# Kernel optimization log

Hardware: AMD Instinct MI355X
Metric: run time of the kernel (lower is better)

The kernel has to match this reference:

```python
import jax, jax.numpy as jnp
import numpy as np

B, S, E, H = 4, 2048, 1024, 16
HD = E // H  # head_dim = 64
EPS = 1.1920928955078125e-07  # torch.finfo(float32).eps (RMSNorm eps=None default)


def _rmsnorm(x, w):
    # normalize over last dim
    ms = jnp.mean(x * x, axis=-1, keepdims=True)
    return x * jax.lax.rsqrt(ms + EPS) * w


def _rope(x, start_pos=0):
    # x: [B, H, S, HD]; interleaved (even/odd) rotary embedding
    seq_len = x.shape[-2]
    inv_freq = 1.0 / (10000.0 ** (jnp.arange(0, HD, 2, dtype=jnp.float32) / HD))  # [HD/2]
    t = jnp.arange(start_pos, start_pos + seq_len, dtype=jnp.float32)  # [S]
    freqs = t[:, None] * inv_freq[None, :]  # [S, HD/2]
    cos = jnp.cos(freqs)[None, None]  # [1,1,S,HD/2]
    sin = jnp.sin(freqs)[None, None]
    x1 = x[..., 0::2]
    x2 = x[..., 1::2]
    o1 = x1 * cos - x2 * sin
    o2 = x1 * sin + x2 * cos
    # stack(..., -1).flatten(-2) -> re-interleave
    return jnp.stack((o1, o2), axis=-1).reshape(x.shape)


def setup_inputs() -> dict:
    key = jax.random.key(0)
    k1, k2, k3, k4 = jax.random.split(key, 4)
    lim = 1.0 / np.sqrt(E)
    return {
        "q": jax.random.normal(k1, (B, S, E), jnp.float32),
        "k": jax.random.normal(k2, (B, S, E), jnp.float32),
        "v": jax.random.normal(k3, (B, S, E), jnp.float32),
        "q_norm_w": jnp.ones((HD,), jnp.float32),
        "k_norm_w": jnp.ones((HD,), jnp.float32),
        "proj_w": jax.random.uniform(k4, (E, E), jnp.float32, -lim, lim),
        "proj_b": jnp.zeros((E,), jnp.float32),
    }


def reference(q, k, v, q_norm_w, k_norm_w, proj_w, proj_b):
    b, s, _ = q.shape
    scale = HD ** -0.5
    # [B,S,E] -> [B,H,S,HD]
    qh = q.reshape(b, s, H, HD).transpose(0, 2, 1, 3)
    kh = k.reshape(b, s, H, HD).transpose(0, 2, 1, 3)
    vh = v.reshape(b, s, H, HD).transpose(0, 2, 1, 3)
    # per-head QK RMSNorm then RoPE
    qh = _rope(_rmsnorm(qh, q_norm_w))
    kh = _rope(_rmsnorm(kh, k_norm_w))
    # explicit attention (no mask path)
    scores = jnp.einsum("bhqd,bhkd->bhqk", qh, kh) * scale  # [B,H,S,S]
    attn = jax.nn.softmax(scores, axis=-1)
    ctx = jnp.einsum("bhqk,bhkd->bhqd", attn, vh)
    ctx = ctx.transpose(0, 2, 1, 3).reshape(b, s, E)
    return ctx @ proj_w.T + proj_b
```

## Files before the change

kernel.cpp:

```cpp
#include <hip/hip_runtime.h>
#include <hip/hip_bf16.h>
#include <cstdint>

#define B_ 4
#define S_ 2048
#define E_ 1024
#define H_ 16
#define HD_ 64
#define EPS_ 1.1920928955078125e-07f

typedef __attribute__((ext_vector_type(8))) short shortx8;
typedef __attribute__((ext_vector_type(4))) float floatx4;
typedef __attribute__((ext_vector_type(8))) _Float16 halfx8;
typedef __attribute__((ext_vector_type(2))) __fp16 fp16x2;

#define C1_ 0.18033688068389154f

__global__ __launch_bounds__(256) void prep(
    const float* __restrict__ q, const float* __restrict__ k,
    const float* __restrict__ v,
    const float* __restrict__ qw, const float* __restrict__ kw,
    const float* __restrict__ pw,
    __hip_bfloat16* __restrict__ qh, __hip_bfloat16* __restrict__ kh,
    _Float16* __restrict__ vt, __hip_bfloat16* __restrict__ wb)
{
    __shared__ _Float16 tile[64][72];
    const int bid = blockIdx.x;
    const int tid = threadIdx.x;

    if (bid < 16384) {
        const size_t PT = (size_t)B_ * S_ * E_ / 4;
        size_t t = (size_t)bid * 256 + tid;
        const bool is_k = (t >= PT);
        if (is_k) t -= PT;

        const int row = (int)(t >> 8);
        const int b   = row / S_;
        const int s   = row % S_;
        const int grp = (int)(t & 255);
        const int h   = grp >> 4;
        const int dl  = (grp & 15) * 4;

        const float* __restrict__ src = is_k ? k : q;
        const float* __restrict__ w   = is_k ? kw : qw;
        __hip_bfloat16* __restrict__ dst = is_k ? kh : qh;

        const float4 x  = ((const float4*)src)[t];
        const float4 wv = ((const float4*)w)[grp & 15];

        float ss = x.x * x.x + x.y * x.y + x.z * x.z + x.w * x.w;
#pragma unroll
        for (int m = 1; m < 16; m <<= 1) ss += __shfl_xor(ss, m);
        float r = rsqrtf(ss * (1.0f / HD_) + EPS_);
        if (!is_k) r *= C1_;

        const float xn0 = x.x * r * wv.x;
        const float xn1 = x.y * r * wv.y;
        const float xn2 = x.z * r * wv.z;
        const float xn3 = x.w * r * wv.w;

        const float L2I = 0.41524101186092029f;
        const int   i0  = dl >> 1;
        const float f0  = (float)s * __builtin_amdgcn_exp2f(-(float)i0 * L2I);
        const float f1  = (float)s * __builtin_amdgcn_exp2f(-(float)(i0 + 1) * L2I);
        const float c0 = __cosf(f0), sn0 = __sinf(f0);
        const float c1 = __cosf(f1), sn1 = __sinf(f1);

        __hip_bfloat16 pk[4];
        pk[0] = __float2bfloat16(xn0 * c0 - xn1 * sn0);
        pk[1] = __float2bfloat16(xn0 * sn0 + xn1 * c0);
        pk[2] = __float2bfloat16(xn2 * c1 - xn3 * sn1);
        pk[3] = __float2bfloat16(xn2 * sn1 + xn3 * c1);
        *(ushort4*)(dst + ((size_t)((b * H_ + h) * S_ + s)) * HD_ + dl) =
            *(const ushort4*)pk;
    } else if (bid < 18432) {
        const int bb2 = bid - 16384;
        const int s0  = (bb2 & 31) * 64;
        const int bh  = bb2 >> 5;
        const int b   = bh >> 4, h = bh & 15;
        {
            const int sl = tid >> 2;
            const int o  = sl;
            const int n  = (o & 32) | (((o >> 2) & 3) << 3) |
                           (((o >> 4) & 1) << 2) | (o & 3);
            const int d0 = (tid & 3) * 16;
            const float* __restrict__ src =
                v + ((size_t)(b * S_ + s0 + sl)) * E_ + h * HD_ + d0;
            float4 f0 = ((const float4*)src)[0];
            float4 f1 = ((const float4*)src)[1];
            float4 f2 = ((const float4*)src)[2];
            float4 f3 = ((const float4*)src)[3];
            float vals[16] = {f0.x,f0.y,f0.z,f0.w, f1.x,f1.y,f1.z,f1.w,
                              f2.x,f2.y,f2.z,f2.w, f3.x,f3.y,f3.z,f3.w};
#pragma unroll
            for (int j = 0; j < 16; ++j)
                tile[d0 + j][n] = (_Float16)vals[j];
        }
        __syncthreads();
        {
            const int d  = tid >> 2;
            const int sg = (tid & 3) * 16;
            _Float16* __restrict__ dst =
                vt + ((size_t)(bh * HD_ + d)) * S_ + s0 + sg;
            ((uint4*)dst)[0] = *(const uint4*)&tile[d][sg];
            ((uint4*)dst)[1] = *(const uint4*)&tile[d][sg + 8];
        }
    } else {
        const int i = (bid - 18432) * 256 + tid;
        float4 f = ((const float4*)pw)[i];
        wb[4 * i + 0] = __float2bfloat16(f.x);
        wb[4 * i + 1] = __float2bfloat16(f.y);
        wb[4 * i + 2] = __float2bfloat16(f.z);
        wb[4 * i + 3] = __float2bfloat16(f.w);
    }
}

__global__ __launch_bounds__(256, 4) void attn(
    const __hip_bfloat16* __restrict__ qh, const __hip_bfloat16* __restrict__ kh,
    const _Float16* __restrict__ vt, __hip_bfloat16* __restrict__ ctx)
{
    __shared__ __hip_bfloat16 Kt[128][72];
    __shared__ _Float16       Vt[64][152];

    const int bid  = blockIdx.x;
    const int slot = bid >> 3;
    const int bh   = ((bid & 7) << 3) | (slot & 7);
    const int q0   = (slot >> 3) * 128;
    const int tid  = threadIdx.x;
    const int wv   = tid >> 6;
    const int lane = tid & 63;
    const int l16  = lane & 15;
    const int quad = lane >> 4;
    const int b    = bh >> 4, h = bh & 15;

    shortx8 aq[2][2];
#pragma unroll
    for (int mh = 0; mh < 2; ++mh) {
        const __hip_bfloat16* qbase =
            qh + ((size_t)bh * S_ + q0 + wv * 32 + mh * 16 + l16) * HD_;
        aq[mh][0] = *(const shortx8*)(qbase + quad * 8);
        aq[mh][1] = *(const shortx8*)(qbase + 32 + quad * 8);
    }

    const halfx8 ones = {(_Float16)1.f, (_Float16)1.f, (_Float16)1.f, (_Float16)1.f,
                         (_Float16)1.f, (_Float16)1.f, (_Float16)1.f, (_Float16)1.f};

    floatx4 O[2][4] = {};
    floatx4 O5[2]   = {};

    const __hip_bfloat16* __restrict__ kbase = kh + (size_t)bh * S_ * HD_;
    const _Float16* __restrict__ vbase = vt + (size_t)bh * HD_ * S_;

    const int sr = tid >> 1, sc = (tid & 1) * 32;
    const int vr = tid >> 2, vc = (tid & 3) * 32;

    for (int kt = 0; kt < S_ / 128; ++kt) {
        {
            const uint4* kp = (const uint4*)(kbase +
                (size_t)(kt * 128 + sr) * HD_ + sc);
            uint4 k0 = kp[0], k1 = kp[1], k2 = kp[2], k3 = kp[3];
            *(uint4*)&Kt[sr][sc]      = k0;
            *(uint4*)&Kt[sr][sc + 8]  = k1;
            *(uint4*)&Kt[sr][sc + 16] = k2;
            *(uint4*)&Kt[sr][sc + 24] = k3;
        }
        {
            const uint4* vp = (const uint4*)(vbase +
                (size_t)vr * S_ + kt * 128 + vc);
            uint4 v0 = vp[0], v1 = vp[1], v2 = vp[2], v3 = vp[3];
            *(uint4*)&Vt[vr][vc]      = v0;
            *(uint4*)&Vt[vr][vc + 8]  = v1;
            *(uint4*)&Vt[vr][vc + 16] = v2;
            *(uint4*)&Vt[vr][vc + 24] = v3;
        }
        __syncthreads();

#pragma unroll
        for (int hk = 0; hk < 2; ++hk) {
            halfx8 bb[2][2];
#pragma unroll
            for (int f = 0; f < 2; ++f) {
                floatx4 s4p[2][2];
                __builtin_amdgcn_s_setprio(1);
#pragma unroll
                for (int nt2 = 0; nt2 < 2; ++nt2) {
                    const int nt = 2 * f + nt2;
                    const shortx8 kb0 =
                        *(const shortx8*)&Kt[hk * 64 + nt * 16 + l16][quad * 8];
                    const shortx8 kb1 =
                        *(const shortx8*)&Kt[hk * 64 + nt * 16 + l16][32 + quad * 8];
#pragma unroll
                    for (int mh = 0; mh < 2; ++mh) {
                        floatx4 c = {0.f, 0.f, 0.f, 0.f};
                        c = __builtin_amdgcn_mfma_f32_16x16x32_bf16(kb0, aq[mh][0], c, 0, 0, 0);
                        c = __builtin_amdgcn_mfma_f32_16x16x32_bf16(kb1, aq[mh][1], c, 0, 0, 0);
                        s4p[mh][nt2] = c;
                    }
                }
                __builtin_amdgcn_s_setprio(0);
#pragma unroll
                for (int mh = 0; mh < 2; ++mh) {
                    union { fp16x2 h2[4]; halfx8 h8; } u;
                    u.h2[0] = __builtin_amdgcn_cvt_pkrtz(
                        __builtin_amdgcn_exp2f(s4p[mh][0][0]),
                        __builtin_amdgcn_exp2f(s4p[mh][0][1]));
                    u.h2[1] = __builtin_amdgcn_cvt_pkrtz(
                        __builtin_amdgcn_exp2f(s4p[mh][0][2]),
                        __builtin_amdgcn_exp2f(s4p[mh][0][3]));
                    u.h2[2] = __builtin_amdgcn_cvt_pkrtz(
                        __builtin_amdgcn_exp2f(s4p[mh][1][0]),
                        __builtin_amdgcn_exp2f(s4p[mh][1][1]));
                    u.h2[3] = __builtin_amdgcn_cvt_pkrtz(
                        __builtin_amdgcn_exp2f(s4p[mh][1][2]),
                        __builtin_amdgcn_exp2f(s4p[mh][1][3]));
                    bb[mh][f] = u.h8;
                }
            }

            __builtin_amdgcn_s_setprio(1);
#pragma unroll
            for (int mh = 0; mh < 2; ++mh) {
                O5[mh] = __builtin_amdgcn_mfma_f32_16x16x32_f16(ones, bb[mh][0], O5[mh], 0, 0, 0);
                O5[mh] = __builtin_amdgcn_mfma_f32_16x16x32_f16(ones, bb[mh][1], O5[mh], 0, 0, 0);
            }

#pragma unroll
            for (int dt = 0; dt < 4; ++dt) {
                const _Float16* vrow = &Vt[dt * 16 + l16][hk * 64];
                const halfx8 A0 = *(const halfx8*)(vrow + quad * 8);
                const halfx8 A1 = *(const halfx8*)(vrow + 32 + quad * 8);
#pragma unroll
                for (int mh = 0; mh < 2; ++mh) {
                    O[mh][dt] = __builtin_amdgcn_mfma_f32_16x16x32_f16(
                        A0, bb[mh][0], O[mh][dt], 0, 0, 0);
                    O[mh][dt] = __builtin_amdgcn_mfma_f32_16x16x32_f16(
                        A1, bb[mh][1], O[mh][dt], 0, 0, 0);
                }
            }
            __builtin_amdgcn_s_setprio(0);
        }
        __syncthreads();
    }

#pragma unroll
    for (int mh = 0; mh < 2; ++mh) {
        const float inv = 1.0f / O5[mh][0];
        const int s = q0 + wv * 32 + mh * 16 + l16;
        __hip_bfloat16* cb = ctx + ((size_t)(b * S_ + s)) * E_ + h * HD_;
#pragma unroll
        for (int dt = 0; dt < 4; ++dt) {
            __hip_bfloat16 pk[4];
#pragma unroll
            for (int r = 0; r < 4; ++r)
                pk[r] = __float2bfloat16(O[mh][dt][r] * inv);
            *(ushort4*)(cb + dt * 16 + quad * 4) = *(const ushort4*)pk;
        }
    }
}

__global__ __launch_bounds__(256) void proj(
    const __hip_bfloat16* __restrict__ ctx, const __hip_bfloat16* __restrict__ wb,
    const float* __restrict__ bias, float* __restrict__ out)
{
    __shared__ __hip_bfloat16 As[128][72];
    __shared__ __hip_bfloat16 Bs[128][72];

    const int bid  = blockIdx.x;
    const int slot = bid >> 3;
    const int mblk = ((bid & 7) << 3) | (slot & 7);
    const int nblk = slot >> 3;
    const int m0 = mblk * 128;
    const int n0 = nblk * 128;
    const int tid  = threadIdx.x;
    const int wv   = tid >> 6;
    const int lane = tid & 63;
    const int l16  = lane & 15;
    const int quad = lane >> 4;
    const int wr   = (wv >> 1) * 64;
    const int wc   = (wv & 1) * 64;

    const int srow = tid >> 1;
    const int scol = (tid & 1) * 32;

    floatx4 acc[4][4] = {};

    for (int k0 = 0; k0 < E_; k0 += 64) {
        const uint4* ap = (const uint4*)(ctx + (size_t)(m0 + srow) * E_ + k0 + scol);
        const uint4* bp = (const uint4*)(wb  + (size_t)(n0 + srow) * E_ + k0 + scol);
        uint4 a0 = ap[0], a1 = ap[1], a2 = ap[2], a3 = ap[3];
        uint4 b0 = bp[0], b1 = bp[1], b2 = bp[2], b3 = bp[3];
        *(uint4*)&As[srow][scol]      = a0;
        *(uint4*)&As[srow][scol + 8]  = a1;
        *(uint4*)&As[srow][scol + 16] = a2;
        *(uint4*)&As[srow][scol + 24] = a3;
        *(uint4*)&Bs[srow][scol]      = b0;
        *(uint4*)&Bs[srow][scol + 8]  = b1;
        *(uint4*)&Bs[srow][scol + 16] = b2;
        *(uint4*)&Bs[srow][scol + 24] = b3;
        __syncthreads();

#pragma unroll
        for (int ks = 0; ks < 2; ++ks) {
            shortx8 af[4], bf[4];
#pragma unroll
            for (int mt = 0; mt < 4; ++mt)
                af[mt] = *(const shortx8*)&As[wr + mt * 16 + l16][ks * 32 + quad * 8];
#pragma unroll
            for (int nt = 0; nt < 4; ++nt)
                bf[nt] = *(const shortx8*)&Bs[wc + nt * 16 + l16][ks * 32 + quad * 8];

#pragma unroll
            for (int mt = 0; mt < 4; ++mt)
#pragma unroll
                for (int nt = 0; nt < 4; ++nt)
                    acc[mt][nt] = __builtin_amdgcn_mfma_f32_16x16x32_bf16(
                        af[mt], bf[nt], acc[mt][nt], 0, 0, 0);
        }
        __syncthreads();
    }

#pragma unroll
    for (int nt = 0; nt < 4; ++nt) {
        const float bv = bias[n0 + wc + nt * 16 + l16];
#pragma unroll
        for (int mt = 0; mt < 4; ++mt)
#pragma unroll
            for (int r = 0; r < 4; ++r) {
                const int mrow = m0 + wr + mt * 16 + quad * 4 + r;
                const int ncol = n0 + wc + nt * 16 + l16;
                out[(size_t)mrow * E_ + ncol] = acc[mt][nt][r] + bv;
            }
    }
}

extern "C" void kernel_launch(void* const* d_in, const int* in_sizes, int n_in,
                              void* d_out, int out_size, void* d_ws, size_t ws_size,
                              hipStream_t stream)
{
    const float* q  = (const float*)d_in[0];
    const float* k  = (const float*)d_in[1];
    const float* v  = (const float*)d_in[2];
    const float* qw = (const float*)d_in[3];
    const float* kw = (const float*)d_in[4];
    const float* pw = (const float*)d_in[5];
    const float* pb = (const float*)d_in[6];
    float* out = (float*)d_out;

    char* ws = (char*)d_ws;
    const size_t SEG = (size_t)B_ * H_ * S_ * HD_ * 2;
    __hip_bfloat16* qh  = (__hip_bfloat16*)(ws);
    __hip_bfloat16* kh  = (__hip_bfloat16*)(ws + SEG);
    _Float16*       vt  = (_Float16*)(ws + 2 * SEG);
    __hip_bfloat16* ctx = (__hip_bfloat16*)(ws + 3 * SEG);
    __hip_bfloat16* wbp = (__hip_bfloat16*)(ws + 4 * SEG);

    prep<<<dim3(19456), 256, 0, stream>>>(q, k, v, qw, kw, pw, qh, kh, vt, wbp);
    attn<<<dim3(1024), 256, 0, stream>>>(qh, kh, vt, ctx);
    proj<<<dim3(512), 256, 0, stream>>>(ctx, wbp, pb, out);
}
```

Measured before the change: 248.1 us.

## Software-pipeline QK, exp and PV stages within each K tile

Replaces the nested hk/f loops with a hand-scheduled sequence that interleaves QK MFMAs, exp2/convert work, and PV MFMAs across four 32-column chunks, so transcendental VALU work overlaps matrix-core work. Also drops the min-blocks-per-CU hint from launch bounds, letting the compiler use more registers for the extra live score buffers. The cost is higher register pressure and possibly lower occupancy.

```diff
diff --git a/kernel.cpp b/kernel.cpp
--- a/kernel.cpp
+++ b/kernel.cpp
@@ -115,7 +115,7 @@
     }
 }
 
-__global__ __launch_bounds__(256, 4) void attn(
+__global__ __launch_bounds__(256) void attn(
     const __hip_bfloat16* __restrict__ qh, const __hip_bfloat16* __restrict__ kh,
     const _Float16* __restrict__ vt, __hip_bfloat16* __restrict__ ctx)
 {
@@ -175,70 +175,88 @@
         }
         __syncthreads();
 
-#pragma unroll
-        for (int hk = 0; hk < 2; ++hk) {
-            halfx8 bb[2][2];
-#pragma unroll
-            for (int f = 0; f < 2; ++f) {
-                floatx4 s4p[2][2];
-                __builtin_amdgcn_s_setprio(1);
-#pragma unroll
-                for (int nt2 = 0; nt2 < 2; ++nt2) {
-                    const int nt = 2 * f + nt2;
-                    const shortx8 kb0 =
-                        *(const shortx8*)&Kt[hk * 64 + nt * 16 + l16][quad * 8];
-                    const shortx8 kb1 =
-                        *(const shortx8*)&Kt[hk * 64 + nt * 16 + l16][32 + quad * 8];
-#pragma unroll
-                    for (int mh = 0; mh < 2; ++mh) {
-                        floatx4 c = {0.f, 0.f, 0.f, 0.f};
-                        c = __builtin_amdgcn_mfma_f32_16x16x32_bf16(kb0, aq[mh][0], c, 0, 0, 0);
-                        c = __builtin_amdgcn_mfma_f32_16x16x32_bf16(kb1, aq[mh][1], c, 0, 0, 0);
-                        s4p[mh][nt2] = c;
-                    }
-                }
-                __builtin_amdgcn_s_setprio(0);
-#pragma unroll
-                for (int mh = 0; mh < 2; ++mh) {
-                    union { fp16x2 h2[4]; halfx8 h8; } u;
-                    u.h2[0] = __builtin_amdgcn_cvt_pkrtz(
-                        __builtin_amdgcn_exp2f(s4p[mh][0][0]),
-                        __builtin_amdgcn_exp2f(s4p[mh][0][1]));
-                    u.h2[1] = __builtin_amdgcn_cvt_pkrtz(
-                        __builtin_amdgcn_exp2f(s4p[mh][0][2]),
-                        __builtin_amdgcn_exp2f(s4p[mh][0][3]));
-                    u.h2[2] = __builtin_amdgcn_cvt_pkrtz(
-                        __builtin_amdgcn_exp2f(s4p[mh][1][0]),
-                        __builtin_amdgcn_exp2f(s4p[mh][1][1]));
-                    u.h2[3] = __builtin_amdgcn_cvt_pkrtz(
-                        __builtin_amdgcn_exp2f(s4p[mh][1][2]),
-                        __builtin_amdgcn_exp2f(s4p[mh][1][3]));
-                    bb[mh][f] = u.h8;
-                }
+        floatx4 sP[2][2], sQ[2][2], sR[2][2], sS[2][2];
+        halfx8 bbA[2], bbB[2], bbC[2], bbD[2];
+
+        auto QKsub = [&](int hk, int nt, floatx4 (&s)[2][2], int nt2) {
+            const shortx8 kb0 =
+                *(const shortx8*)&Kt[hk * 64 + nt * 16 + l16][quad * 8];
+            const shortx8 kb1 =
+                *(const shortx8*)&Kt[hk * 64 + nt * 16 + l16][32 + quad * 8];
+#pragma unroll
+            for (int mh = 0; mh < 2; ++mh) {
+                floatx4 c = {0.f, 0.f, 0.f, 0.f};
+                c = __builtin_amdgcn_mfma_f32_16x16x32_bf16(kb0, aq[mh][0], c, 0, 0, 0);
+                c = __builtin_amdgcn_mfma_f32_16x16x32_bf16(kb1, aq[mh][1], c, 0, 0, 0);
+                s[mh][nt2] = c;
             }
-
-            __builtin_amdgcn_s_setprio(1);
-#pragma unroll
-            for (int mh = 0; mh < 2; ++mh) {
-                O5[mh] = __builtin_amdgcn_mfma_f32_16x16x32_f16(ones, bb[mh][0], O5[mh], 0, 0, 0);
-                O5[mh] = __builtin_amdgcn_mfma_f32_16x16x32_f16(ones, bb[mh][1], O5[mh], 0, 0, 0);
-            }
-
-#pragma unroll
-            for (int dt = 0; dt < 4; ++dt) {
-                const _Float16* vrow = &Vt[dt * 16 + l16][hk * 64];
-                const halfx8 A0 = *(const halfx8*)(vrow + quad * 8);
-                const halfx8 A1 = *(const halfx8*)(vrow + 32 + quad * 8);
-#pragma unroll
-                for (int mh = 0; mh < 2; ++mh) {
-                    O[mh][dt] = __builtin_amdgcn_mfma_f32_16x16x32_f16(
-                        A0, bb[mh][0], O[mh][dt], 0, 0, 0);
-                    O[mh][dt] = __builtin_amdgcn_mfma_f32_16x16x32_f16(
-                        A1, bb[mh][1], O[mh][dt], 0, 0, 0);
-                }
-            }
-            __builtin_amdgcn_s_setprio(0);
-        }
+        };
+        auto EXPmh = [&](const floatx4& s0, const floatx4& s1, halfx8& dst) {
+            union { fp16x2 h2[4]; halfx8 h8; } u;
+            u.h2[0] = __builtin_amdgcn_cvt_pkrtz(
+                __builtin_amdgcn_exp2f(s0[0]), __builtin_amdgcn_exp2f(s0[1]));
+            u.h2[1] = __builtin_amdgcn_cvt_pkrtz(
+                __builtin_amdgcn_exp2f(s0[2]), __builtin_amdgcn_exp2f(s0[3]));
+            u.h2[2] = __builtin_amdgcn_cvt_pkrtz(
+                __builtin_amdgcn_exp2f(s1[0]), __builtin_amdgcn_exp2f(s1[1]));
+            u.h2[3] = __builtin_amdgcn_cvt_pkrtz(
+                __builtin_amdgcn_exp2f(s1[2]), __builtin_amdgcn_exp2f(s1[3]));
+            dst = u.h8;
+        };
+        auto Lacc = [&](halfx8 (&bb)[2]) {
+#pragma unroll
+            for (int mh = 0; mh < 2; ++mh)
+                O5[mh] = __builtin_amdgcn_mfma_f32_16x16x32_f16(
+                    ones, bb[mh], O5[mh], 0, 0, 0);
+        };
+        auto PVdt = [&](int hk, int half, int dt, halfx8 (&bb)[2]) {
+            const _Float16* vrow = &Vt[dt * 16 + l16][hk * 64];
+            const halfx8 A = *(const halfx8*)(vrow + half * 32 + quad * 8);
+#pragma unroll
+            for (int mh = 0; mh < 2; ++mh)
+                O[mh][dt] = __builtin_amdgcn_mfma_f32_16x16x32_f16(
+                    A, bb[mh], O[mh][dt], 0, 0, 0);
+        };
+
+        __builtin_amdgcn_s_setprio(1);
+        QKsub(0, 0, sP, 0);
+        QKsub(0, 1, sP, 1);
+        QKsub(0, 2, sQ, 0);
+        EXPmh(sP[0][0], sP[0][1], bbA[0]);
+        QKsub(0, 3, sQ, 1);
+        EXPmh(sP[1][0], sP[1][1], bbA[1]);
+        QKsub(1, 0, sR, 0);
+        EXPmh(sQ[0][0], sQ[0][1], bbB[0]);
+        QKsub(1, 1, sR, 1);
+        EXPmh(sQ[1][0], sQ[1][1], bbB[1]);
+        Lacc(bbA);
+        PVdt(0, 0, 0, bbA);
+        EXPmh(sR[0][0], sR[0][1], bbC[0]);
+        PVdt(0, 0, 1, bbA);
+        PVdt(0, 0, 2, bbA);
+        EXPmh(sR[1][0], sR[1][1], bbC[1]);
+        PVdt(0, 0, 3, bbA);
+        QKsub(1, 2, sS, 0);
+        QKsub(1, 3, sS, 1);
+        Lacc(bbB);
+        PVdt(0, 1, 0, bbB);
+        EXPmh(sS[0][0], sS[0][1], bbD[0]);
+        PVdt(0, 1, 1, bbB);
+        PVdt(0, 1, 2, bbB);
+        EXPmh(sS[1][0], sS[1][1], bbD[1]);
+        PVdt(0, 1, 3, bbB);
+        Lacc(bbC);
+        PVdt(1, 0, 0, bbC);
+        PVdt(1, 0, 1, bbC);
+        PVdt(1, 0, 2, bbC);
+        PVdt(1, 0, 3, bbC);
+        Lacc(bbD);
+        PVdt(1, 1, 0, bbD);
+        PVdt(1, 1, 1, bbD);
+        PVdt(1, 1, 2, bbD);
+        PVdt(1, 1, 3, bbD);
+        __builtin_amdgcn_s_setprio(0);
+
         __syncthreads();
     }
 
```

Measured after the change: 267.5 us. 1.08x slower.

## Double-buffer K/V shared tiles and drop trailing barrier in attention loop

Applied to the files above, without the earlier changes.

Splits the K and V shared-memory tiles into two alternating buffers indexed by iteration parity, so the end-of-iteration barrier can be removed and only one barrier per key tile remains. The minimum-blocks-per-CU launch hint is dropped. The cost is roughly double the LDS per block, which reduces how many blocks can reside on a CU and may lower latency hiding.

```diff
diff --git a/kernel.cpp b/kernel.cpp
--- a/kernel.cpp
+++ b/kernel.cpp
@@ -115,12 +115,12 @@
     }
 }
 
-__global__ __launch_bounds__(256, 4) void attn(
+__global__ __launch_bounds__(256) void attn(
     const __hip_bfloat16* __restrict__ qh, const __hip_bfloat16* __restrict__ kh,
     const _Float16* __restrict__ vt, __hip_bfloat16* __restrict__ ctx)
 {
-    __shared__ __hip_bfloat16 Kt[128][72];
-    __shared__ _Float16       Vt[64][152];
+    __shared__ __hip_bfloat16 Kt[2][128][72];
+    __shared__ _Float16       Vt[2][64][152];
 
     const int bid  = blockIdx.x;
     const int slot = bid >> 3;
@@ -155,23 +155,24 @@
     const int vr = tid >> 2, vc = (tid & 3) * 32;
 
     for (int kt = 0; kt < S_ / 128; ++kt) {
+        const int pb = kt & 1;
         {
             const uint4* kp = (const uint4*)(kbase +
                 (size_t)(kt * 128 + sr) * HD_ + sc);
             uint4 k0 = kp[0], k1 = kp[1], k2 = kp[2], k3 = kp[3];
-            *(uint4*)&Kt[sr][sc]      = k0;
-            *(uint4*)&Kt[sr][sc + 8]  = k1;
-            *(uint4*)&Kt[sr][sc + 16] = k2;
-            *(uint4*)&Kt[sr][sc + 24] = k3;
+            *(uint4*)&Kt[pb][sr][sc]      = k0;
+            *(uint4*)&Kt[pb][sr][sc + 8]  = k1;
+            *(uint4*)&Kt[pb][sr][sc + 16] = k2;
+            *(uint4*)&Kt[pb][sr][sc + 24] = k3;
         }
         {
             const uint4* vp = (const uint4*)(vbase +
                 (size_t)vr * S_ + kt * 128 + vc);
             uint4 v0 = vp[0], v1 = vp[1], v2 = vp[2], v3 = vp[3];
-            *(uint4*)&Vt[vr][vc]      = v0;
-            *(uint4*)&Vt[vr][vc + 8]  = v1;
-            *(uint4*)&Vt[vr][vc + 16] = v2;
-            *(uint4*)&Vt[vr][vc + 24] = v3;
+            *(uint4*)&Vt[pb][vr][vc]      = v0;
+            *(uint4*)&Vt[pb][vr][vc + 8]  = v1;
+            *(uint4*)&Vt[pb][vr][vc + 16] = v2;
+            *(uint4*)&Vt[pb][vr][vc + 24] = v3;
         }
         __syncthreads();
 
@@ -186,9 +187,9 @@
                 for (int nt2 = 0; nt2 < 2; ++nt2) {
                     const int nt = 2 * f + nt2;
                     const shortx8 kb0 =
-                        *(const shortx8*)&Kt[hk * 64 + nt * 16 + l16][quad * 8];
+                        *(const shortx8*)&Kt[pb][hk * 64 + nt * 16 + l16][quad * 8];
                     const shortx8 kb1 =
-                        *(const shortx8*)&Kt[hk * 64 + nt * 16 + l16][32 + quad * 8];
+                        *(const shortx8*)&Kt[pb][hk * 64 + nt * 16 + l16][32 + quad * 8];
 #pragma unroll
                     for (int mh = 0; mh < 2; ++mh) {
                         floatx4 c = {0.f, 0.f, 0.f, 0.f};
@@ -226,7 +227,7 @@
 
 #pragma unroll
             for (int dt = 0; dt < 4; ++dt) {
-                const _Float16* vrow = &Vt[dt * 16 + l16][hk * 64];
+                const _Float16* vrow = &Vt[pb][dt * 16 + l16][hk * 64];
                 const halfx8 A0 = *(const halfx8*)(vrow + quad * 8);
                 const halfx8 A1 = *(const halfx8*)(vrow + 32 + quad * 8);
 #pragma unroll
@@ -239,7 +240,6 @@
             }
             __builtin_amdgcn_s_setprio(0);
         }
-        __syncthreads();
     }
 
 #pragma unroll
```

New measurement: 258.9 us. +4.4%, slower.
